# Optimization experiments

Hardware: AMD Instinct MI355X
Metric: run time of the kernel (lower is better)

Reference implementation:

```python
import jax, jax.numpy as jnp
import numpy as np

D = 1024      # features
C = 768       # context dim
H = 16        # heads
HD = D // H   # head dim = 64
N = 2048      # query tokens
M = 2048      # context tokens
EPS = 1e-12
SCALE = float(np.sqrt(HD))


def layernorm(x, w, b):
    c = x - x.mean(axis=-1, keepdims=True)
    s = (c * c).mean(axis=-1, keepdims=True)
    return c * jax.lax.rsqrt(s + EPS) * w + b


def setup_inputs() -> dict:
    key = jax.random.key(0)
    ks = jax.random.split(key, 10)
    sc = 0.02
    return {
        "x": jax.random.normal(ks[0], (N, D), jnp.float32),
        "ctx": jax.random.normal(ks[1], (M, C), jnp.float32),
        # attention projections (Projection: normal*0.02, zero bias)
        "wq": jax.random.normal(ks[2], (D, D), jnp.float32) * sc,
        "bq": jnp.zeros((D,), jnp.float32),
        "wk": jax.random.normal(ks[3], (C, D), jnp.float32) * sc,
        "bk": jnp.zeros((D,), jnp.float32),
        "wv": jax.random.normal(ks[4], (C, D), jnp.float32) * sc,
        "bv": jnp.zeros((D,), jnp.float32),
        "wo": jax.random.normal(ks[5], (D, D), jnp.float32) * sc,
        "bo": jnp.zeros((D,), jnp.float32),
        # MLP
        "w1": jax.random.normal(ks[6], (D, 4 * D), jnp.float32) * sc,
        "b1": jnp.zeros((4 * D,), jnp.float32),
        "w2": jax.random.normal(ks[7], (4 * D, D), jnp.float32) * sc,
        "b2": jnp.zeros((D,), jnp.float32),
        # layernorms
        "qn_w": jnp.ones((D,), jnp.float32), "qn_b": jnp.zeros((D,), jnp.float32),
        "kvn_w": jnp.ones((C,), jnp.float32), "kvn_b": jnp.zeros((C,), jnp.float32),
        "pn_w": jnp.ones((D,), jnp.float32), "pn_b": jnp.zeros((D,), jnp.float32),
    }


def reference(x, ctx, wq, bq, wk, bk, wv, bv, wo, bo, w1, b1, w2, b2,
              qn_w, qn_b, kvn_w, kvn_b, pn_w, pn_b):
    # pre-norm cross-attention
    xq = layernorm(x, qn_w, qn_b)          # [n, d]
    kv = layernorm(ctx, kvn_w, kvn_b)      # [m, c]
    q = (xq @ wq + bq).reshape(N, H, HD).transpose(1, 0, 2)   # [h, n, hd]
    k = (kv @ wk + bk).reshape(M, H, HD).transpose(1, 0, 2)   # [h, m, hd]
    v = (kv @ wv + bv).reshape(M, H, HD).transpose(1, 0, 2)   # [h, m, hd]
    attn = jax.nn.softmax(jnp.einsum('hnd,hmd->hnm', q, k) / SCALE, axis=-1)
    o = jnp.einsum('hnm,hmd->hnd', attn, v).transpose(1, 0, 2).reshape(N, D)
    x = (o @ wo + bo) + x
    # MLP block
    h = layernorm(x, pn_w, pn_b)
    h = jax.nn.gelu(h @ w1 + b1) @ w2 + b2
    return h + x
```

## Files before the change

kernel.cpp:

```cpp
#include <hip/hip_runtime.h>

typedef __bf16 bf16;
typedef __bf16 bf16x4 __attribute__((ext_vector_type(4)));
typedef __bf16 bf16x8 __attribute__((ext_vector_type(8)));
typedef float f32x4 __attribute__((ext_vector_type(4)));

#define N_TOK 2048
#define M_TOK 2048
#define DIM 1024
#define CDIM 768
#define DFF 4096

static __device__ __forceinline__ void async16(const void* g, void* l) {
  __builtin_amdgcn_global_load_lds((const __attribute__((address_space(1))) void*)g,
                                   (__attribute__((address_space(3))) void*)l, 16, 0, 0);
}

__global__ __launch_bounds__(256) void detect_kernel(const void* x, int* flag) {
  __shared__ int cnt;
  if (threadIdx.x == 0) cnt = 0;
  __syncthreads();
  const unsigned* w = (const unsigned*)x;
  int ok = 0;
  for (int i = threadIdx.x; i < 512; i += 256) {
    unsigned lo = w[i] & 0xFFFFu;
    float f = __uint_as_float(lo << 16);
    if (lo == 0u || (fabsf(f) > 1e-3f && fabsf(f) < 1e3f)) ok++;
  }
  atomicAdd(&cnt, ok);
  __syncthreads();
  if (threadIdx.x == 0) *flag = (cnt >= 256) ? 1 : 0;
}

struct ConvArgs {
  const void* src[12];
  bf16* dst[12];
  int n[12];
};
__global__ __launch_bounds__(256) void conv_small_kernel(ConvArgs a, const int* flag) {
  const bool isbf = (*flag != 0);
  const int b = blockIdx.x;
  const void* in = a.src[b];
  bf16* out = a.dst[b];
  const int n = a.n[b];
  for (int i = threadIdx.x; i < n; i += 256)
    out[i] = isbf ? ((const bf16*)in)[i] : (bf16)((const float*)in)[i];
}

struct TmArgs {
  const void* src[4];
  bf16* dst[4];
  int r0[4], Rcnt[4], c0[4], Cfull[4], gx[4], gy[4];
  int force_bf;
};
__global__ __launch_bounds__(256) void tmulti_kernel(TmArgs a, const int* flag) {
  const int z = blockIdx.z;
  if ((int)blockIdx.x >= a.gx[z] || (int)blockIdx.y >= a.gy[z]) return;
  __shared__ bf16 t[32][33];
  const bool isbf = a.force_bf || (*flag != 0);
  const void* in = a.src[z];
  bf16* out = a.dst[z];
  const int Rcnt = a.Rcnt[z], Cfull = a.Cfull[z];
  const int cb = blockIdx.x * 32, rb = blockIdx.y * 32;
  const int tx = threadIdx.x & 31, ty = threadIdx.x >> 5;
#pragma unroll
  for (int i = 0; i < 4; i++) {
    const size_t r = (size_t)(a.r0[z] + rb + ty + i * 8);
    const size_t c = (size_t)(a.c0[z] + cb + tx);
    float v = isbf ? (float)((const bf16*)in)[r * Cfull + c]
                   : ((const float*)in)[r * Cfull + c];
    t[ty + i * 8][tx] = (bf16)v;
  }
  __syncthreads();
#pragma unroll
  for (int i = 0; i < 4; i++)
    out[(size_t)(cb + ty + i * 8) * Rcnt + rb + tx] = t[tx][ty + i * 8];
}

__global__ __launch_bounds__(256) void ln_pair_kernel(
    const void* __restrict__ x0, const bf16* w0, const bf16* b0, bf16* o0,
    const void* __restrict__ x1, const bf16* w1, const bf16* b1, bf16* o1,
    const int* flag) {
  const bool isbf = (*flag != 0);
  const int cols = (blockIdx.y == 0) ? DIM : CDIM;
  const void* x = (blockIdx.y == 0) ? x0 : x1;
  const bf16* w = (blockIdx.y == 0) ? w0 : w1;
  const bf16* b = (blockIdx.y == 0) ? b0 : b1;
  bf16* outp = (blockIdx.y == 0) ? o0 : o1;
  const int row = blockIdx.x;
  const bf16* xr_b = (const bf16*)x + (size_t)row * cols;
  const float* xr_f = (const float*)x + (size_t)row * cols;
  bf16* orow = outp + (size_t)row * cols;
  float s = 0.f, ss = 0.f;
  for (int c = threadIdx.x; c < cols; c += 256) {
    float v = isbf ? (float)xr_b[c] : xr_f[c];
    s += v; ss += v * v;
  }
  for (int d = 1; d < 64; d <<= 1) { s += __shfl_xor(s, d, 64); ss += __shfl_xor(ss, d, 64); }
  __shared__ float sh[8];
  const int wv = threadIdx.x >> 6, lane = threadIdx.x & 63;
  if (lane == 0) { sh[wv] = s; sh[4 + wv] = ss; }
  __syncthreads();
  s = sh[0] + sh[1] + sh[2] + sh[3];
  ss = sh[4] + sh[5] + sh[6] + sh[7];
  const float mean = s / cols;
  float var = ss / cols - mean * mean;
  var = fmaxf(var, 0.f);
  const float r = rsqrtf(var + 1e-12f);
  for (int c = threadIdx.x; c < cols; c += 256) {
    float v = isbf ? (float)xr_b[c] : xr_f[c];
    orow[c] = (bf16)((v - mean) * r * (float)w[c] + (float)b[c]);
  }
}

__global__ __launch_bounds__(256) void ln_kernel(
    const bf16* __restrict__ x, const bf16* __restrict__ w, const bf16* __restrict__ b,
    bf16* __restrict__ out, int cols) {
  const int row = blockIdx.x;
  const bf16* xr = x + (size_t)row * cols;
  bf16* orow = out + (size_t)row * cols;
  float s = 0.f, ss = 0.f;
  for (int c = threadIdx.x; c < cols; c += 256) {
    float v = (float)xr[c];
    s += v; ss += v * v;
  }
  for (int d = 1; d < 64; d <<= 1) { s += __shfl_xor(s, d, 64); ss += __shfl_xor(ss, d, 64); }
  __shared__ float sh[8];
  const int wv = threadIdx.x >> 6, lane = threadIdx.x & 63;
  if (lane == 0) { sh[wv] = s; sh[4 + wv] = ss; }
  __syncthreads();
  s = sh[0] + sh[1] + sh[2] + sh[3];
  ss = sh[4] + sh[5] + sh[6] + sh[7];
  const float mean = s / cols;
  float var = ss / cols - mean * mean;
  var = fmaxf(var, 0.f);
  const float r = rsqrtf(var + 1e-12f);
  for (int c = threadIdx.x; c < cols; c += 256) {
    float v = (float)xr[c];
    orow[c] = (bf16)((v - mean) * r * (float)w[c] + (float)b[c]);
  }
}

__device__ __forceinline__ float gelu_f(float x) {
  float u = 0.7978845608028654f * (x + 0.044715f * x * x * x);
  return 0.5f * x * (1.f + tanhf(u));
}

template <int EPI>
__global__ __launch_bounds__(256) void gemm64(
    const bf16* __restrict__ A, const bf16* __restrict__ Bt,
    const bf16* __restrict__ bias, const void* __restrict__ resid,
    void* __restrict__ Cout, int K, int ldc, const int* flag) {
  __shared__ __align__(16) bf16 As[4][64 * 32];
  __shared__ __align__(16) bf16 Bs[4][64 * 32];
  const int tid = threadIdx.x;
  const int lane = tid & 63, wv = tid >> 6;
  const int lq = lane >> 4, lm = lane & 15;
  const int row0 = blockIdx.y * 64, col0 = blockIdx.x * 64;
  const int wr = (wv >> 1) * 32, wc = (wv & 1) * 32;

  f32x4 acc[2][2] = {};
  const int r_a = wv * 16 + (lane >> 2);
  const int kc = (lane & 3) * 8;

  for (int k0 = 0; k0 < K; k0 += 128) {
    __syncthreads();
#pragma unroll
    for (int b = 0; b < 4; b++) {
      async16(A + (size_t)(row0 + r_a) * K + k0 + b * 32 + kc, As[b] + wv * 512);
      async16(Bt + (size_t)(col0 + r_a) * K + k0 + b * 32 + kc, Bs[b] + wv * 512);
    }
    __syncthreads();
#pragma unroll
    for (int b = 0; b < 4; b++) {
      bf16x8 af[2], bfv[2];
#pragma unroll
      for (int t = 0; t < 2; t++)
        af[t] = *(const bf16x8*)&As[b][(wr + t * 16 + lm) * 32 + lq * 8];
#pragma unroll
      for (int t = 0; t < 2; t++)
        bfv[t] = *(const bf16x8*)&Bs[b][(wc + t * 16 + lm) * 32 + lq * 8];
#pragma unroll
      for (int i = 0; i < 2; i++)
#pragma unroll
        for (int j = 0; j < 2; j++)
          acc[i][j] = __builtin_amdgcn_mfma_f32_16x16x32_bf16(af[i], bfv[j], acc[i][j], 0, 0, 0);
    }
  }

  const bool isbf = (*flag != 0);
#pragma unroll
  for (int i = 0; i < 2; i++) {
    const int rb = row0 + wr + i * 16 + lq * 4;
#pragma unroll
    for (int j = 0; j < 2; j++) {
      const int c = col0 + wc + j * 16 + lm;
      const float bv = (EPI != 5) ? (float)bias[c] : 0.f;
#pragma unroll
      for (int rg = 0; rg < 4; rg++) {
        const size_t idx = (size_t)(rb + rg) * ldc + c;
        float v = acc[i][j][rg] + bv;
        if (EPI == 1)
          v += isbf ? (float)((const bf16*)resid)[idx] : ((const float*)resid)[idx];
        if (EPI == 2) v = gelu_f(v);
        if (EPI == 4) v += (float)((const bf16*)resid)[idx];
        if (EPI == 5)
          v += isbf ? (float)((bf16*)Cout)[idx] : ((float*)Cout)[idx];
        if (EPI == 4 || EPI == 5) {
          if (isbf) ((bf16*)Cout)[idx] = (bf16)v;
          else      ((float*)Cout)[idx] = v;
        } else {
          ((bf16*)Cout)[idx] = (bf16)v;
        }
      }
    }
  }
}

struct QkvArgs {
  const bf16* A[3];
  const bf16* Bt[3];
  const bf16* bias[3];
  bf16* C[3];
  int K[3], ldc[3], gx[3], gy[3], brow[3];
};
__global__ __launch_bounds__(256) void gemm64_qkv(QkvArgs a) {
  const int z = blockIdx.z;
  if ((int)blockIdx.x >= a.gx[z] || (int)blockIdx.y >= a.gy[z]) return;
  const bf16* A = a.A[z];
  const bf16* Bt = a.Bt[z];
  const int K = a.K[z];
  __shared__ __align__(16) bf16 As[4][64 * 32];
  __shared__ __align__(16) bf16 Bs[4][64 * 32];
  const int tid = threadIdx.x;
  const int lane = tid & 63, wv = tid >> 6;
  const int lq = lane >> 4, lm = lane & 15;
  const int row0 = blockIdx.y * 64, col0 = blockIdx.x * 64;
  const int wr = (wv >> 1) * 32, wc = (wv & 1) * 32;

  f32x4 acc[2][2] = {};
  const int r_a = wv * 16 + (lane >> 2);
  const int kc = (lane & 3) * 8;

  for (int k0 = 0; k0 < K; k0 += 128) {
    __syncthreads();
#pragma unroll
    for (int b = 0; b < 4; b++) {
      async16(A + (size_t)(row0 + r_a) * K + k0 + b * 32 + kc, As[b] + wv * 512);
      async16(Bt + (size_t)(col0 + r_a) * K + k0 + b * 32 + kc, Bs[b] + wv * 512);
    }
    __syncthreads();
#pragma unroll
    for (int b = 0; b < 4; b++) {
      bf16x8 af[2], bfv[2];
#pragma unroll
      for (int t = 0; t < 2; t++)
        af[t] = *(const bf16x8*)&As[b][(wr + t * 16 + lm) * 32 + lq * 8];
#pragma unroll
      for (int t = 0; t < 2; t++)
        bfv[t] = *(const bf16x8*)&Bs[b][(wc + t * 16 + lm) * 32 + lq * 8];
#pragma unroll
      for (int i = 0; i < 2; i++)
#pragma unroll
        for (int j = 0; j < 2; j++)
          acc[i][j] = __builtin_amdgcn_mfma_f32_16x16x32_bf16(af[i], bfv[j], acc[i][j], 0, 0, 0);
    }
  }

  const bf16* bias = a.bias[z];
  bf16* C = a.C[z];
  const int ldc = a.ldc[z];
  const bool brow = a.brow[z] != 0;
#pragma unroll
  for (int i = 0; i < 2; i++) {
    const int rb = row0 + wr + i * 16 + lq * 4;
#pragma unroll
    for (int j = 0; j < 2; j++) {
      const int c = col0 + wc + j * 16 + lm;
      const float bcol = brow ? 0.f : (float)bias[c];
#pragma unroll
      for (int rg = 0; rg < 4; rg++) {
        const float bv = brow ? (float)bias[rb + rg] : bcol;
        C[(size_t)(rb + rg) * ldc + c] = (bf16)(acc[i][j][rg] + bv);
      }
    }
  }
}

#define KS_STR 72
#define VS_STR 136
__global__ __launch_bounds__(256) void attn_kernel(
    const bf16* __restrict__ q, const bf16* __restrict__ k,
    const bf16* __restrict__ vT, bf16* __restrict__ pO0, bf16* __restrict__ pO1,
    float* __restrict__ l0, float* __restrict__ l1) {
  __shared__ __align__(16) bf16 KPs[128 * KS_STR];
  __shared__ __align__(16) bf16 Vs[64 * VS_STR];
  const int tid = threadIdx.x, lane = tid & 63, wv = tid >> 6;
  const int lq = lane >> 4, lm = lane & 15;
  const int h = blockIdx.y;
  const int n0 = blockIdx.x * 64;
  const int half = blockIdx.z;
  const int mbeg = half * (M_TOK / 2), mend = mbeg + M_TOK / 2;
  bf16* pO = half ? pO1 : pO0;
  float* lb = half ? l1 : l0;

  bf16x8 qf[2];
#pragma unroll
  for (int f = 0; f < 2; f++)
    qf[f] = *(const bf16x8*)&q[(size_t)(n0 + wv * 16 + lm) * DIM + h * 64 + f * 32 + lq * 8];

  f32x4 oacc[4] = {};
  float lsum = 0.f;
  const float sc = 0.125f * 1.4426950408889634f;

  for (int m0 = mbeg; m0 < mend; m0 += 128) {
    __syncthreads();
#pragma unroll
    for (int it = 0; it < 4; it++) {
      const int e = tid * 8 + it * 2048;
      const int r = e >> 6, c = e & 63;
      *(bf16x8*)&KPs[r * KS_STR + c] =
          *(const bf16x8*)&k[(size_t)(m0 + r) * DIM + h * 64 + c];
    }
#pragma unroll
    for (int it = 0; it < 4; it++) {
      const int e = tid * 8 + it * 2048;
      const int r = e >> 7, c = e & 127;
      *(bf16x8*)&Vs[r * VS_STR + c] =
          *(const bf16x8*)&vT[(size_t)(h * 64 + r) * M_TOK + m0 + c];
    }
    __syncthreads();

    f32x4 s[8];
#pragma unroll
    for (int j = 0; j < 8; j++) {
      bf16x8 kf0 = *(const bf16x8*)&KPs[(j * 16 + lm) * KS_STR + lq * 8];
      bf16x8 kf1 = *(const bf16x8*)&KPs[(j * 16 + lm) * KS_STR + 32 + lq * 8];
      f32x4 z = {};
      z = __builtin_amdgcn_mfma_f32_16x16x32_bf16(kf0, qf[0], z, 0, 0, 0);
      s[j] = __builtin_amdgcn_mfma_f32_16x16x32_bf16(kf1, qf[1], z, 0, 0, 0);
    }
    __syncthreads();

#pragma unroll
    for (int j = 0; j < 8; j++) {
      bf16x4 pw;
#pragma unroll
      for (int rg = 0; rg < 4; rg++) {
        const float pv = exp2f(s[j][rg] * sc);
        lsum += pv;
        pw[rg] = (bf16)pv;
      }
      *(bf16x4*)&KPs[(wv * 16 + lm) * VS_STR + j * 16 + lq * 4] = pw;
    }

#pragma unroll
    for (int kk = 0; kk < 4; kk++) {
      bf16x8 pf = *(const bf16x8*)&KPs[(wv * 16 + lm) * VS_STR + kk * 32 + lq * 8];
#pragma unroll
      for (int dt = 0; dt < 4; dt++) {
        bf16x8 vf = *(const bf16x8*)&Vs[(dt * 16 + lm) * VS_STR + kk * 32 + lq * 8];
        oacc[dt] = __builtin_amdgcn_mfma_f32_16x16x32_bf16(vf, pf, oacc[dt], 0, 0, 0);
      }
    }
  }

  lsum += __shfl_xor(lsum, 16, 64);
  lsum += __shfl_xor(lsum, 32, 64);
  if (lane < 16) lb[h * N_TOK + n0 + wv * 16 + lane] = lsum;

  const int rn = n0 + wv * 16 + lm;
#pragma unroll
  for (int dt = 0; dt < 4; dt++) {
    bf16x4 ow;
#pragma unroll
    for (int rg = 0; rg < 4; rg++) ow[rg] = (bf16)oacc[dt][rg];
    *(bf16x4*)&pO[(size_t)rn * DIM + h * 64 + dt * 16 + lq * 4] = ow;
  }
}

__global__ __launch_bounds__(256) void attn_combine(
    const bf16* __restrict__ pO0, const bf16* __restrict__ pO1,
    const float* __restrict__ l0, const float* __restrict__ l1,
    bf16* __restrict__ om) {
  const int i4 = (blockIdx.x * 256 + threadIdx.x) * 4;
  const int n = i4 >> 10;
  const int h = (i4 & 1023) >> 6;
  const float rinv = 1.f / (l0[h * N_TOK + n] + l1[h * N_TOK + n]);
  bf16x4 a = *(const bf16x4*)&pO0[i4];
  bf16x4 b = *(const bf16x4*)&pO1[i4];
  bf16x4 o;
#pragma unroll
  for (int r = 0; r < 4; r++) o[r] = (bf16)(((float)a[r] + (float)b[r]) * rinv);
  *(bf16x4*)&om[i4] = o;
}

extern "C" void kernel_launch(void* const* d_in, const int* in_sizes, int n_in,
                              void* d_out, int out_size, void* d_ws, size_t ws_size,
                              hipStream_t stream) {
  const void* x_r     = d_in[0];
  const void* ctx_r   = d_in[1];
  const void* wq_r    = d_in[2];
  const void* bq_r    = d_in[3];
  const void* wk_r    = d_in[4];
  const void* bk_r    = d_in[5];
  const void* wv_r    = d_in[6];
  const void* bv_r    = d_in[7];
  const void* wo_r    = d_in[8];
  const void* bo_r    = d_in[9];
  const void* w1_r    = d_in[10];
  const void* b1_r    = d_in[11];
  const void* w2_r    = d_in[12];
  const void* b2_r    = d_in[13];
  const void* qnw_r   = d_in[14];
  const void* qnb_r   = d_in[15];
  const void* kvnw_r  = d_in[16];
  const void* kvnb_r  = d_in[17];
  const void* pnw_r   = d_in[18];
  const void* pnb_r   = d_in[19];

  bf16* p = (bf16*)d_ws;
  const size_t MEG = 1024 * 1024;
  bf16* qm  = p;             bf16* hln = qm;
  bf16* km  = p + 2 * MEG;   bf16* xat = km;
  bf16* wC  = p + 4 * MEG;
  bf16* xq  = p + 8 * MEG;   bf16* pO0 = xq;   bf16* om = xq;
  bf16* vTb = p + 10 * MEG;
  bf16* kvn = p + 12 * MEG;  bf16* pO1 = kvn;
  bf16* h1h = p + 10 * MEG;
  bf16* SM  = p + 14 * MEG;
  int* flag = (int*)(p + 14 * MEG + 16384);

  bf16* wqT = wC;
  bf16* wkT = wC + 1 * MEG;
  bf16* wvT = wC + 1 * MEG + 786432;
  bf16* woT = wC + 2 * MEG + 524288;
  bf16* w1Th = wC;
  bf16* w2Th = wC + 2 * MEG;
  float* l0 = (float*)wC;
  float* l1 = l0 + N_TOK * 16;

  bf16* bqc = SM, *bkc = SM + 1024, *bvc = SM + 2048, *boc = SM + 3072;
  bf16* b1c = SM + 4096, *b2c = SM + 8192;
  bf16* qnw = SM + 9216, *qnb = SM + 10240;
  bf16* kvnw = SM + 11264, *kvnb = SM + 12032;
  bf16* pnw = SM + 12800, *pnb = SM + 13824;

  detect_kernel<<<1, 256, 0, stream>>>(x_r, flag);
  ConvArgs ca;
  ca.src[0] = bq_r;   ca.dst[0] = bqc;  ca.n[0] = DIM;
  ca.src[1] = bk_r;   ca.dst[1] = bkc;  ca.n[1] = DIM;
  ca.src[2] = bv_r;   ca.dst[2] = bvc;  ca.n[2] = DIM;
  ca.src[3] = bo_r;   ca.dst[3] = boc;  ca.n[3] = DIM;
  ca.src[4] = b1_r;   ca.dst[4] = b1c;  ca.n[4] = DFF;
  ca.src[5] = b2_r;   ca.dst[5] = b2c;  ca.n[5] = DIM;
  ca.src[6] = qnw_r;  ca.dst[6] = qnw;  ca.n[6] = DIM;
  ca.src[7] = qnb_r;  ca.dst[7] = qnb;  ca.n[7] = DIM;
  ca.src[8] = kvnw_r; ca.dst[8] = kvnw; ca.n[8] = CDIM;
  ca.src[9] = kvnb_r; ca.dst[9] = kvnb; ca.n[9] = CDIM;
  ca.src[10] = pnw_r; ca.dst[10] = pnw; ca.n[10] = DIM;
  ca.src[11] = pnb_r; ca.dst[11] = pnb; ca.n[11] = DIM;
  conv_small_kernel<<<12, 256, 0, stream>>>(ca, flag);

  ln_pair_kernel<<<dim3(2048, 2), 256, 0, stream>>>(x_r, qnw, qnb, xq,
                                                    ctx_r, kvnw, kvnb, kvn, flag);

  {
    TmArgs ta;
    ta.force_bf = 0;
    ta.src[0] = wq_r; ta.dst[0] = wqT; ta.r0[0] = 0; ta.Rcnt[0] = DIM;
    ta.c0[0] = 0; ta.Cfull[0] = DIM; ta.gx[0] = 32; ta.gy[0] = 32;
    ta.src[1] = wk_r; ta.dst[1] = wkT; ta.r0[1] = 0; ta.Rcnt[1] = CDIM;
    ta.c0[1] = 0; ta.Cfull[1] = DIM; ta.gx[1] = 32; ta.gy[1] = 24;
    ta.src[2] = wv_r; ta.dst[2] = wvT; ta.r0[2] = 0; ta.Rcnt[2] = CDIM;
    ta.c0[2] = 0; ta.Cfull[2] = DIM; ta.gx[2] = 32; ta.gy[2] = 24;
    ta.src[3] = wo_r; ta.dst[3] = woT; ta.r0[3] = 0; ta.Rcnt[3] = DIM;
    ta.c0[3] = 0; ta.Cfull[3] = DIM; ta.gx[3] = 32; ta.gy[3] = 32;
    tmulti_kernel<<<dim3(32, 32, 4), 256, 0, stream>>>(ta, flag);
  }

  {
    QkvArgs qa;
    qa.A[0] = xq;  qa.Bt[0] = wqT; qa.bias[0] = bqc; qa.C[0] = qm;
    qa.K[0] = DIM;  qa.ldc[0] = DIM;   qa.gx[0] = 16; qa.gy[0] = 32; qa.brow[0] = 0;
    qa.A[1] = kvn; qa.Bt[1] = wkT; qa.bias[1] = bkc; qa.C[1] = km;
    qa.K[1] = CDIM; qa.ldc[1] = DIM;   qa.gx[1] = 16; qa.gy[1] = 32; qa.brow[1] = 0;
    qa.A[2] = wvT; qa.Bt[2] = kvn; qa.bias[2] = bvc; qa.C[2] = vTb;
    qa.K[2] = CDIM; qa.ldc[2] = M_TOK; qa.gx[2] = 32; qa.gy[2] = 16; qa.brow[2] = 1;
    gemm64_qkv<<<dim3(32, 32, 3), 256, 0, stream>>>(qa);
  }

  attn_kernel<<<dim3(32, 16, 2), 256, 0, stream>>>(qm, km, vTb, pO0, pO1, l0, l1);
  attn_combine<<<2048, 256, 0, stream>>>(pO0, pO1, l0, l1, om);

  gemm64<1><<<dim3(16, 32), 256, 0, stream>>>(om, woT, boc, x_r, xat, DIM, DIM, flag);

  ln_kernel<<<N_TOK, 256, 0, stream>>>(xat, pnw, pnb, hln, DIM);

  for (int hh = 0; hh < 2; hh++) {
    TmArgs ta;
    ta.force_bf = 0;
    ta.src[0] = w1_r; ta.dst[0] = w1Th; ta.r0[0] = 0; ta.Rcnt[0] = DIM;
    ta.c0[0] = hh * 2048; ta.Cfull[0] = DFF; ta.gx[0] = 64; ta.gy[0] = 32;
    ta.src[1] = w2_r; ta.dst[1] = w2Th; ta.r0[1] = hh * 2048; ta.Rcnt[1] = 2048;
    ta.c0[1] = 0; ta.Cfull[1] = DIM; ta.gx[1] = 32; ta.gy[1] = 64;
    ta.src[2] = ta.src[0]; ta.dst[2] = ta.dst[0]; ta.r0[2] = 0; ta.Rcnt[2] = 32;
    ta.c0[2] = 0; ta.Cfull[2] = DIM; ta.gx[2] = 0; ta.gy[2] = 0;
    ta.src[3] = ta.src[0]; ta.dst[3] = ta.dst[0]; ta.r0[3] = 0; ta.Rcnt[3] = 32;
    ta.c0[3] = 0; ta.Cfull[3] = DIM; ta.gx[3] = 0; ta.gy[3] = 0;
    tmulti_kernel<<<dim3(64, 64, 2), 256, 0, stream>>>(ta, flag);

    gemm64<2><<<dim3(32, 32), 256, 0, stream>>>(hln, w1Th, b1c + hh * 2048, nullptr,
                                                h1h, DIM, 2048, flag);
    if (hh == 0)
      gemm64<4><<<dim3(16, 32), 256, 0, stream>>>(h1h, w2Th, b2c, xat, d_out,
                                                  2048, DIM, flag);
    else
      gemm64<5><<<dim3(16, 32), 256, 0, stream>>>(h1h, w2Th, b2c, nullptr, d_out,
                                                  2048, DIM, flag);
  }
}
```

Before: 354.6 us.

## Widen GEMM tiles to 64x128 and double query rows per attention block

Adds a 64x128-tile GEMM (gemm_bt2) used for the QKV projections and the GELU up-projection, so each warp computes a 32x64 output with 2x4 MFMA tiles. Each K-step shrinks from 128 to 64, and the GELU epilogue moves out of gemm64 into the new kernel. The attention kernel now processes 128 query rows per block (32 per warp), reusing each K/V LDS tile across two query sub-tiles, and LDS strides change. The aim is more compute per shared-memory load and fewer global reloads, at the cost of more registers, fewer blocks, and possible LDS bank conflicts from the new strides.

After: 361.4 us. No clear change (+1.9%).

```diff
diff --git a/kernel.cpp b/kernel.cpp
--- a/kernel.cpp
+++ b/kernel.cpp
@@ -202,7 +202,6 @@
         float v = acc[i][j][rg] + bv;
         if (EPI == 1)
           v += isbf ? (float)((const bf16*)resid)[idx] : ((const float*)resid)[idx];
-        if (EPI == 2) v = gelu_f(v);
         if (EPI == 4) v += (float)((const bf16*)resid)[idx];
         if (EPI == 5)
           v += isbf ? (float)((bf16*)Cout)[idx] : ((float*)Cout)[idx];
@@ -217,6 +216,67 @@
   }
 }
 
+template <int EPI>
+__global__ __launch_bounds__(256) void gemm_bt2(
+    const bf16* __restrict__ A, const bf16* __restrict__ Bt,
+    const bf16* __restrict__ bias, bf16* __restrict__ C, int K, int ldc) {
+  __shared__ __align__(16) bf16 As[2][64 * 32];
+  __shared__ __align__(16) bf16 Bs[2][128 * 32];
+  const int tid = threadIdx.x;
+  const int lane = tid & 63, wv = tid >> 6;
+  const int lq = lane >> 4, lm = lane & 15;
+  const int row0 = blockIdx.y * 64, col0 = blockIdx.x * 128;
+  const int wr = (wv >> 1) * 32, wc = (wv & 1) * 64;
+
+  f32x4 acc[2][4] = {};
+  const int r_a = wv * 16 + (lane >> 2);
+  const int kc = (lane & 3) * 8;
+
+  for (int k0 = 0; k0 < K; k0 += 64) {
+    __syncthreads();
+#pragma unroll
+    for (int b = 0; b < 2; b++) {
+      async16(A + (size_t)(row0 + r_a) * K + k0 + b * 32 + kc, As[b] + wv * 512);
+#pragma unroll
+      for (int i = 0; i < 2; i++)
+        async16(Bt + (size_t)(col0 + wv * 32 + i * 16 + (lane >> 2)) * K + k0 + b * 32 + kc,
+                Bs[b] + wv * 1024 + i * 512);
+    }
+    __syncthreads();
+#pragma unroll
+    for (int b = 0; b < 2; b++) {
+      bf16x8 af[2], bfv[4];
+#pragma unroll
+      for (int t = 0; t < 2; t++)
+        af[t] = *(const bf16x8*)&As[b][(wr + t * 16 + lm) * 32 + lq * 8];
+#pragma unroll
+      for (int u = 0; u < 4; u++)
+        bfv[u] = *(const bf16x8*)&Bs[b][(wc + u * 16 + lm) * 32 + lq * 8];
+#pragma unroll
+      for (int t = 0; t < 2; t++)
+#pragma unroll
+        for (int u = 0; u < 4; u++)
+          acc[t][u] = __builtin_amdgcn_mfma_f32_16x16x32_bf16(af[t], bfv[u], acc[t][u], 0, 0, 0);
+    }
+  }
+
+#pragma unroll
+  for (int t = 0; t < 2; t++) {
+    const int rb = row0 + wr + t * 16 + lq * 4;
+#pragma unroll
+    for (int u = 0; u < 4; u++) {
+      const int c = col0 + wc + u * 16 + lm;
+      const float bv = (float)bias[c];
+#pragma unroll
+      for (int rg = 0; rg < 4; rg++) {
+        float v = acc[t][u][rg] + bv;
+        if (EPI == 2) v = gelu_f(v);
+        C[(size_t)(rb + rg) * ldc + c] = (bf16)v;
+      }
+    }
+  }
+}
+
 struct QkvArgs {
   const bf16* A[3];
   const bf16* Bt[3];
@@ -224,46 +284,49 @@
   bf16* C[3];
   int K[3], ldc[3], gx[3], gy[3], brow[3];
 };
-__global__ __launch_bounds__(256) void gemm64_qkv(QkvArgs a) {
+__global__ __launch_bounds__(256) void gemm_bt2_qkv(QkvArgs a) {
   const int z = blockIdx.z;
   if ((int)blockIdx.x >= a.gx[z] || (int)blockIdx.y >= a.gy[z]) return;
   const bf16* A = a.A[z];
   const bf16* Bt = a.Bt[z];
   const int K = a.K[z];
-  __shared__ __align__(16) bf16 As[4][64 * 32];
-  __shared__ __align__(16) bf16 Bs[4][64 * 32];
+  __shared__ __align__(16) bf16 As[2][64 * 32];
+  __shared__ __align__(16) bf16 Bs[2][128 * 32];
   const int tid = threadIdx.x;
   const int lane = tid & 63, wv = tid >> 6;
   const int lq = lane >> 4, lm = lane & 15;
-  const int row0 = blockIdx.y * 64, col0 = blockIdx.x * 64;
-  const int wr = (wv >> 1) * 32, wc = (wv & 1) * 32;
-
-  f32x4 acc[2][2] = {};
+  const int row0 = blockIdx.y * 64, col0 = blockIdx.x * 128;
+  const int wr = (wv >> 1) * 32, wc = (wv & 1) * 64;
+
+  f32x4 acc[2][4] = {};
   const int r_a = wv * 16 + (lane >> 2);
   const int kc = (lane & 3) * 8;
 
-  for (int k0 = 0; k0 < K; k0 += 128) {
-    __syncthreads();
-#pragma unroll
-    for (int b = 0; b < 4; b++) {
+  for (int k0 = 0; k0 < K; k0 += 64) {
+    __syncthreads();
+#pragma unroll
+    for (int b = 0; b < 2; b++) {
       async16(A + (size_t)(row0 + r_a) * K + k0 + b * 32 + kc, As[b] + wv * 512);
-      async16(Bt + (size_t)(col0 + r_a) * K + k0 + b * 32 + kc, Bs[b] + wv * 512);
-    }
-    __syncthreads();
-#pragma unroll
-    for (int b = 0; b < 4; b++) {
-      bf16x8 af[2], bfv[2];
+#pragma unroll
+      for (int i = 0; i < 2; i++)
+        async16(Bt + (size_t)(col0 + wv * 32 + i * 16 + (lane >> 2)) * K + k0 + b * 32 + kc,
+                Bs[b] + wv * 1024 + i * 512);
+    }
+    __syncthreads();
+#pragma unroll
+    for (int b = 0; b < 2; b++) {
+      bf16x8 af[2], bfv[4];
 #pragma unroll
       for (int t = 0; t < 2; t++)
         af[t] = *(const bf16x8*)&As[b][(wr + t * 16 + lm) * 32 + lq * 8];
 #pragma unroll
+      for (int u = 0; u < 4; u++)
+        bfv[u] = *(const bf16x8*)&Bs[b][(wc + u * 16 + lm) * 32 + lq * 8];
+#pragma unroll
       for (int t = 0; t < 2; t++)
-        bfv[t] = *(const bf16x8*)&Bs[b][(wc + t * 16 + lm) * 32 + lq * 8];
-#pragma unroll
-      for (int i = 0; i < 2; i++)
-#pragma unroll
-        for (int j = 0; j < 2; j++)
-          acc[i][j] = __builtin_amdgcn_mfma_f32_16x16x32_bf16(af[i], bfv[j], acc[i][j], 0, 0, 0);
+#pragma unroll
+        for (int u = 0; u < 4; u++)
+          acc[t][u] = __builtin_amdgcn_mfma_f32_16x16x32_bf16(af[t], bfv[u], acc[t][u], 0, 0, 0);
     }
   }
 
@@ -272,45 +335,48 @@
   const int ldc = a.ldc[z];
   const bool brow = a.brow[z] != 0;
 #pragma unroll
-  for (int i = 0; i < 2; i++) {
-    const int rb = row0 + wr + i * 16 + lq * 4;
-#pragma unroll
-    for (int j = 0; j < 2; j++) {
-      const int c = col0 + wc + j * 16 + lm;
+  for (int t = 0; t < 2; t++) {
+    const int rb = row0 + wr + t * 16 + lq * 4;
+#pragma unroll
+    for (int u = 0; u < 4; u++) {
+      const int c = col0 + wc + u * 16 + lm;
       const float bcol = brow ? 0.f : (float)bias[c];
 #pragma unroll
       for (int rg = 0; rg < 4; rg++) {
         const float bv = brow ? (float)bias[rb + rg] : bcol;
-        C[(size_t)(rb + rg) * ldc + c] = (bf16)(acc[i][j][rg] + bv);
+        C[(size_t)(rb + rg) * ldc + c] = (bf16)(acc[t][u][rg] + bv);
       }
     }
   }
 }
 
-#define KS_STR 72
-#define VS_STR 136
+#define KS_STR 68
+#define PS_STR 132
 __global__ __launch_bounds__(256) void attn_kernel(
     const bf16* __restrict__ q, const bf16* __restrict__ k,
     const bf16* __restrict__ vT, bf16* __restrict__ pO0, bf16* __restrict__ pO1,
     float* __restrict__ l0, float* __restrict__ l1) {
-  __shared__ __align__(16) bf16 KPs[128 * KS_STR];
-  __shared__ __align__(16) bf16 Vs[64 * VS_STR];
+  __shared__ __align__(16) bf16 KPs[128 * PS_STR];
+  __shared__ __align__(16) bf16 Vs[64 * PS_STR];
   const int tid = threadIdx.x, lane = tid & 63, wv = tid >> 6;
   const int lq = lane >> 4, lm = lane & 15;
   const int h = blockIdx.y;
-  const int n0 = blockIdx.x * 64;
+  const int n0 = blockIdx.x * 128;
   const int half = blockIdx.z;
   const int mbeg = half * (M_TOK / 2), mend = mbeg + M_TOK / 2;
   bf16* pO = half ? pO1 : pO0;
   float* lb = half ? l1 : l0;
 
-  bf16x8 qf[2];
-#pragma unroll
-  for (int f = 0; f < 2; f++)
-    qf[f] = *(const bf16x8*)&q[(size_t)(n0 + wv * 16 + lm) * DIM + h * 64 + f * 32 + lq * 8];
-
-  f32x4 oacc[4] = {};
-  float lsum = 0.f;
+  bf16x8 qf[2][2];
+#pragma unroll
+  for (int ns = 0; ns < 2; ns++)
+#pragma unroll
+    for (int f = 0; f < 2; f++)
+      qf[ns][f] = *(const bf16x8*)
+          &q[(size_t)(n0 + wv * 32 + ns * 16 + lm) * DIM + h * 64 + f * 32 + lq * 8];
+
+  f32x4 oacc[2][4] = {};
+  float lsum[2] = {0.f, 0.f};
   const float sc = 0.125f * 1.4426950408889634f;
 
   for (int m0 = mbeg; m0 < mend; m0 += 128) {
@@ -326,56 +392,75 @@
     for (int it = 0; it < 4; it++) {
       const int e = tid * 8 + it * 2048;
       const int r = e >> 7, c = e & 127;
-      *(bf16x8*)&Vs[r * VS_STR + c] =
+      *(bf16x8*)&Vs[r * PS_STR + c] =
           *(const bf16x8*)&vT[(size_t)(h * 64 + r) * M_TOK + m0 + c];
     }
     __syncthreads();
 
-    f32x4 s[8];
+    f32x4 s[2][8];
 #pragma unroll
     for (int j = 0; j < 8; j++) {
       bf16x8 kf0 = *(const bf16x8*)&KPs[(j * 16 + lm) * KS_STR + lq * 8];
       bf16x8 kf1 = *(const bf16x8*)&KPs[(j * 16 + lm) * KS_STR + 32 + lq * 8];
-      f32x4 z = {};
-      z = __builtin_amdgcn_mfma_f32_16x16x32_bf16(kf0, qf[0], z, 0, 0, 0);
-      s[j] = __builtin_amdgcn_mfma_f32_16x16x32_bf16(kf1, qf[1], z, 0, 0, 0);
-    }
-    __syncthreads();
-
-#pragma unroll
-    for (int j = 0; j < 8; j++) {
-      bf16x4 pw;
-#pragma unroll
-      for (int rg = 0; rg < 4; rg++) {
-        const float pv = exp2f(s[j][rg] * sc);
-        lsum += pv;
-        pw[rg] = (bf16)pv;
+#pragma unroll
+      for (int ns = 0; ns < 2; ns++) {
+        f32x4 z = {};
+        z = __builtin_amdgcn_mfma_f32_16x16x32_bf16(kf0, qf[ns][0], z, 0, 0, 0);
+        s[ns][j] = __builtin_amdgcn_mfma_f32_16x16x32_bf16(kf1, qf[ns][1], z, 0, 0, 0);
       }
-      *(bf16x4*)&KPs[(wv * 16 + lm) * VS_STR + j * 16 + lq * 4] = pw;
-    }
+    }
+    __syncthreads();
+
+#pragma unroll
+    for (int ns = 0; ns < 2; ns++)
+#pragma unroll
+      for (int j = 0; j < 8; j++) {
+        bf16x4 pw;
+#pragma unroll
+        for (int rg = 0; rg < 4; rg++) {
+          const float pv = exp2f(s[ns][j][rg] * sc);
+          lsum[ns] += pv;
+          pw[rg] = (bf16)pv;
+        }
+        *(bf16x4*)&KPs[(wv * 32 + ns * 16 + lm) * PS_STR + j * 16 + lq * 4] = pw;
+      }
 
 #pragma unroll
     for (int kk = 0; kk < 4; kk++) {
-      bf16x8 pf = *(const bf16x8*)&KPs[(wv * 16 + lm) * VS_STR + kk * 32 + lq * 8];
-#pragma unroll
-      for (int dt = 0; dt < 4; dt++) {
-        bf16x8 vf = *(const bf16x8*)&Vs[(dt * 16 + lm) * VS_STR + kk * 32 + lq * 8];
-        oacc[dt] = __builtin_amdgcn_mfma_f32_16x16x32_bf16(vf, pf, oacc[dt], 0, 0, 0);
+      bf16x8 vf[4];
+#pragma unroll
+      for (int dt = 0; dt < 4; dt++)
+        vf[dt] = *(const bf16x8*)&Vs[(dt * 16 + lm) * PS_STR + kk * 32 + lq * 8];
+#pragma unroll
+      for (int ns = 0; ns < 2; ns++) {
+        bf16x8 pf = *(const bf16x8*)&KPs[(wv * 32 + ns * 16 + lm) * PS_STR + kk * 32 + lq * 8];
+#pragma unroll
+        for (int dt = 0; dt < 4; dt++)
+          oacc[ns][dt] = __builtin_amdgcn_mfma_f32_16x16x32_bf16(vf[dt], pf, oacc[ns][dt], 0, 0, 0);
       }
     }
   }
 
-  lsum += __shfl_xor(lsum, 16, 64);
-  lsum += __shfl_xor(lsum, 32, 64);
-  if (lane < 16) lb[h * N_TOK + n0 + wv * 16 + lane] = lsum;
-
-  const int rn = n0 + wv * 16 + lm;
-#pragma unroll
-  for (int dt = 0; dt < 4; dt++) {
-    bf16x4 ow;
-#pragma unroll
-    for (int rg = 0; rg < 4; rg++) ow[rg] = (bf16)oacc[dt][rg];
-    *(bf16x4*)&pO[(size_t)rn * DIM + h * 64 + dt * 16 + lq * 4] = ow;
+#pragma unroll
+  for (int ns = 0; ns < 2; ns++) {
+    lsum[ns] += __shfl_xor(lsum[ns], 16, 64);
+    lsum[ns] += __shfl_xor(lsum[ns], 32, 64);
+  }
+  if (lane < 16) {
+    lb[h * N_TOK + n0 + wv * 32 + lane] = lsum[0];
+    lb[h * N_TOK + n0 + wv * 32 + 16 + lane] = lsum[1];
+  }
+
+#pragma unroll
+  for (int ns = 0; ns < 2; ns++) {
+    const int rn = n0 + wv * 32 + ns * 16 + lm;
+#pragma unroll
+    for (int dt = 0; dt < 4; dt++) {
+      bf16x4 ow;
+#pragma unroll
+      for (int rg = 0; rg < 4; rg++) ow[rg] = (bf16)oacc[ns][dt][rg];
+      *(bf16x4*)&pO[(size_t)rn * DIM + h * 64 + dt * 16 + lq * 4] = ow;
+    }
   }
 }
 
@@ -482,15 +567,15 @@
   {
     QkvArgs qa;
     qa.A[0] = xq;  qa.Bt[0] = wqT; qa.bias[0] = bqc; qa.C[0] = qm;
-    qa.K[0] = DIM;  qa.ldc[0] = DIM;   qa.gx[0] = 16; qa.gy[0] = 32; qa.brow[0] = 0;
+    qa.K[0] = DIM;  qa.ldc[0] = DIM;   qa.gx[0] = 8;  qa.gy[0] = 32; qa.brow[0] = 0;
     qa.A[1] = kvn; qa.Bt[1] = wkT; qa.bias[1] = bkc; qa.C[1] = km;
-    qa.K[1] = CDIM; qa.ldc[1] = DIM;   qa.gx[1] = 16; qa.gy[1] = 32; qa.brow[1] = 0;
+    qa.K[1] = CDIM; qa.ldc[1] = DIM;   qa.gx[1] = 8;  qa.gy[1] = 32; qa.brow[1] = 0;
     qa.A[2] = wvT; qa.Bt[2] = kvn; qa.bias[2] = bvc; qa.C[2] = vTb;
-    qa.K[2] = CDIM; qa.ldc[2] = M_TOK; qa.gx[2] = 32; qa.gy[2] = 16; qa.brow[2] = 1;
-    gemm64_qkv<<<dim3(32, 32, 3), 256, 0, stream>>>(qa);
-  }
-
-  attn_kernel<<<dim3(32, 16, 2), 256, 0, stream>>>(qm, km, vTb, pO0, pO1, l0, l1);
+    qa.K[2] = CDIM; qa.ldc[2] = M_TOK; qa.gx[2] = 16; qa.gy[2] = 16; qa.brow[2] = 1;
+    gemm_bt2_qkv<<<dim3(16, 32, 3), 256, 0, stream>>>(qa);
+  }
+
+  attn_kernel<<<dim3(16, 16, 2), 256, 0, stream>>>(qm, km, vTb, pO0, pO1, l0, l1);
   attn_combine<<<2048, 256, 0, stream>>>(pO0, pO1, l0, l1, om);
 
   gemm64<1><<<dim3(16, 32), 256, 0, stream>>>(om, woT, boc, x_r, xat, DIM, DIM, flag);
@@ -510,8 +595,8 @@
     ta.c0[3] = 0; ta.Cfull[3] = DIM; ta.gx[3] = 0; ta.gy[3] = 0;
     tmulti_kernel<<<dim3(64, 64, 2), 256, 0, stream>>>(ta, flag);
 
-    gemm64<2><<<dim3(32, 32), 256, 0, stream>>>(hln, w1Th, b1c + hh * 2048, nullptr,
-                                                h1h, DIM, 2048, flag);
+    gemm_bt2<2><<<dim3(16, 32), 256, 0, stream>>>(hln, w1Th, b1c + hh * 2048, h1h,
+                                                  DIM, 2048);
     if (hh == 0)
       gemm64<4><<<dim3(16, 32), 256, 0, stream>>>(h1h, w2Th, b2c, xat, d_out,
                                                   2048, DIM, flag);
```
